# Kernel tuning notes

Measured on AMD Instinct MI355X. Metric: run time of the kernel, lower is better.

The kernel has to match this reference:

```python
import jax, jax.numpy as jnp
import numpy as np

KL_W = 0.001
DENSITY_W = 0.1
SIZING_W = 0.05
BIG = 1e6


def _pairwise_sqdist(x, y):
    # x: [B,N,3], y: [B,M,3] -> [B,N,M] squared euclidean distances
    x2 = jnp.sum(x * x, axis=-1)  # [B,N]
    y2 = jnp.sum(y * y, axis=-1)  # [B,M]
    xy = jnp.einsum('bnd,bmd->bnm', x, y)
    return x2[:, :, None] + y2[:, None, :] - 2.0 * xy


def setup_inputs() -> dict:
    key = jax.random.key(0)
    ks = jax.random.split(key, 6)
    B, N, D, L = 4, 4096, 3, 512
    return {
        'pred_pos': jax.random.normal(ks[0], (B, N, D), dtype=jnp.float32),
        'pred_sizing': jax.random.uniform(ks[1], (B, N), dtype=jnp.float32),
        'target_pos': jax.random.normal(ks[2], (B, N, D), dtype=jnp.float32),
        'target_sizing': jax.random.uniform(ks[3], (B, N), dtype=jnp.float32),
        'mu': jax.random.normal(ks[4], (B, L), dtype=jnp.float32),
        'logvar': jax.random.normal(ks[5], (B, L), dtype=jnp.float32),
    }


def reference(pred_pos, pred_sizing, target_pos, target_sizing, mu, logvar):
    # Chamfer distance (bidirectional)
    dist = _pairwise_sqdist(pred_pos, target_pos)  # [B,N,M]
    d_p2t = jnp.min(dist, axis=2).mean(axis=1)     # [B]
    d_t2p = jnp.min(dist, axis=1).mean(axis=1)     # [B]
    cd = jnp.mean(d_p2t + d_t2p)

    # KL divergence term
    kl = -0.5 * jnp.mean(1.0 + logvar - mu * mu - jnp.exp(logvar))

    # Density uniformity: std (ddof=1, torch default) of nearest-neighbor sq-dist
    N = pred_pos.shape[1]
    d_self = _pairwise_sqdist(pred_pos, pred_pos)
    d_self = d_self + jnp.eye(N, dtype=d_self.dtype)[None] * BIG
    nn_d = jnp.min(d_self, axis=2)                 # [B,N]
    density = jnp.mean(jnp.std(nn_d, axis=1, ddof=1))

    # Sizing MSE
    sizing = jnp.mean((pred_sizing - target_sizing) ** 2)

    total = cd + KL_W * kl + DENSITY_W * density + SIZING_W * sizing
    return total
```

## Files before the change

kernel.cpp:

```cpp
#include <hip/hip_runtime.h>
#include <cfloat>
#include <cmath>

#define NB     4
#define NPTS   4096
#define NLAT   512
#define RPTS   8
#define CJ     64
#define NJC    (NPTS / CJ)
#define NIH    2

__global__ __launch_bounds__(256) void k_prep(
    const float* __restrict__ pred_pos, const float* __restrict__ targ_pos,
    float4* __restrict__ predT, float4* __restrict__ predR,
    float4* __restrict__ targT, float4* __restrict__ targR)
{
    const int i = blockIdx.x * 256 + threadIdx.x;
    {
        const float x = pred_pos[3*i], y = pred_pos[3*i+1], z = pred_pos[3*i+2];
        const float p2 = fmaf(z, z, fmaf(y, y, x * x));
        predT[i] = make_float4(-2.f*x, -2.f*y, -2.f*z, p2);
        predR[i] = make_float4(x, y, z, p2);
    }
    {
        const float x = targ_pos[3*i], y = targ_pos[3*i+1], z = targ_pos[3*i+2];
        const float p2 = fmaf(z, z, fmaf(y, y, x * x));
        targT[i] = make_float4(-2.f*x, -2.f*y, -2.f*z, p2);
        targR[i] = make_float4(x, y, z, p2);
    }
}

__global__ __launch_bounds__(256) void k_min_dist(
    const float4* __restrict__ predT, const float4* __restrict__ predR,
    const float4* __restrict__ targT, const float4* __restrict__ targR,
    float* __restrict__ part_mins )
{
    __shared__ float4 lds[CJ];

    const int tid   = threadIdx.x;
    const int jc    = blockIdx.x & (NJC - 1);
    const int ihalf = (blockIdx.x >> 6) & 1;
    const int b     = (blockIdx.x >> 7) & 3;
    const int mode  = blockIdx.x >> 9;

    const float4* iR = ((mode == 1) ? targR : predR) + (size_t)b * NPTS;
    const float4* jT = ((mode == 0) ? targT : predT) + (size_t)b * NPTS + jc * CJ;

    if (tid < CJ) lds[tid] = jT[tid];

    float px[RPTS], py[RPTS], pz[RPTS], p2[RPTS], acc[RPTS];
    #pragma unroll
    for (int k = 0; k < RPTS; ++k) {
        const float4 r = iR[ihalf * 2048 + (k << 8) + tid];
        px[k] = r.x; py[k] = r.y; pz[k] = r.z; p2[k] = r.w;
        acc[k] = FLT_MAX;
    }
    __syncthreads();

    if (mode != 2) {
        #pragma unroll 2
        for (int j = 0; j < CJ; j += 2) {
            const float4 o1 = lds[j];
            const float4 o2 = lds[j + 1];
            #pragma unroll
            for (int k = 0; k < RPTS; ++k) {
                float t1 = fmaf(o1.x, px[k], o1.w);
                t1 = fmaf(o1.y, py[k], t1);
                t1 = fmaf(o1.z, pz[k], t1);
                float t2 = fmaf(o2.x, px[k], o2.w);
                t2 = fmaf(o2.y, py[k], t2);
                t2 = fmaf(o2.z, pz[k], t2);
                acc[k] = fminf(acc[k], fminf(t1, t2));
            }
        }
    } else {
        const bool have = (jc >> 5) == ihalf;
        const int  kself = (jc & 31) >> 2;
        const bool aff   = have && ((tid >> 6) == (jc & 3));
        const int  jself = tid & 63;
        float sx = px[0], sy = py[0], sz = pz[0];
        #pragma unroll
        for (int k = 1; k < RPTS; ++k) {
            sx = (k == kself) ? px[k] : sx;
            sy = (k == kself) ? py[k] : sy;
            sz = (k == kself) ? pz[k] : sz;
        }
        float accf = FLT_MAX;
        #pragma unroll 2
        for (int j = 0; j < CJ; j += 2) {
            const float4 o1 = lds[j];
            const float4 o2 = lds[j + 1];
            #pragma unroll
            for (int k = 0; k < RPTS; ++k) {
                float t1 = fmaf(o1.x, px[k], o1.w);
                t1 = fmaf(o1.y, py[k], t1);
                t1 = fmaf(o1.z, pz[k], t1);
                float t2 = fmaf(o2.x, px[k], o2.w);
                t2 = fmaf(o2.y, py[k], t2);
                t2 = fmaf(o2.z, pz[k], t2);
                acc[k] = fminf(acc[k], fminf(t1, t2));
            }
            float f1 = fmaf(o1.x, sx, o1.w);
            f1 = fmaf(o1.y, sy, f1);
            f1 = fmaf(o1.z, sz, f1);
            f1 = (j == jself) ? FLT_MAX : f1;
            float f2 = fmaf(o2.x, sx, o2.w);
            f2 = fmaf(o2.y, sy, f2);
            f2 = fmaf(o2.z, sz, f2);
            f2 = ((j + 1) == jself) ? FLT_MAX : f2;
            accf = fminf(accf, fminf(f1, f2));
        }
        #pragma unroll
        for (int k = 0; k < RPTS; ++k)
            acc[k] = (aff && k == kself) ? accf : acc[k];
    }

    float* mb = part_mins + (((size_t)mode * NB + b) * NJC + jc) * NPTS
                + ihalf * 2048;
    #pragma unroll
    for (int k = 0; k < RPTS; ++k)
        mb[(k << 8) + tid] = acc[k] + p2[k];
}

__device__ __forceinline__ float block_sum(float v, float* red)
{
    #pragma unroll
    for (int o = 32; o >= 1; o >>= 1) v += __shfl_xor(v, o);
    const int w = threadIdx.x >> 6;
    __syncthreads();
    if ((threadIdx.x & 63) == 0) red[w] = v;
    __syncthreads();
    return red[0] + red[1] + red[2] + red[3];
}

__global__ __launch_bounds__(256) void k_fold(
    const float* __restrict__ part_mins,
    const float* __restrict__ pred_sizing,
    const float* __restrict__ targ_sizing,
    const float* __restrict__ mu,
    const float* __restrict__ logvar,
    float* __restrict__ sums ,
    float* __restrict__ sumsqs )
{
    __shared__ float red[4];
    const int blk = blockIdx.x, tid = threadIdx.x;

    if (blk < 192) {
        const int slice = blk & 15;
        const int b     = (blk >> 4) & 3;
        const int mode  = blk >> 6;
        const float* base = part_mins + ((size_t)mode * NB + b) * NJC * NPTS
                            + slice * 256 + tid;
        float m = FLT_MAX;
        #pragma unroll 8
        for (int jc = 0; jc < NJC; ++jc)
            m = fminf(m, base[(size_t)jc * NPTS]);
        const float s  = block_sum(m, red);
        const float s2 = block_sum(m * m, red);
        if (tid == 0) { sums[blk] = s; sumsqs[blk] = s2; }
    } else if (blk == 192) {
        float kls = 0.f;
        for (int i = tid; i < NB * NLAT; i += 256) {
            const float lv = logvar[i], m = mu[i];
            kls += 1.f + lv - m * m - expf(lv);
        }
        kls = block_sum(kls, red);
        if (tid == 0) { sums[192] = kls; sumsqs[192] = 0.f; }
    } else {
        const float4* ps = (const float4*)pred_sizing;
        const float4* ts = (const float4*)targ_sizing;
        float szs = 0.f;
        #pragma unroll 4
        for (int i = tid; i < NB * NPTS / 4; i += 256) {
            const float4 a = ps[i], c = ts[i];
            const float d0 = a.x - c.x, d1 = a.y - c.y;
            const float d2 = a.z - c.z, d3 = a.w - c.w;
            szs += fmaf(d0, d0, fmaf(d1, d1, fmaf(d2, d2, d3 * d3)));
        }
        szs = block_sum(szs, red);
        if (tid == 0) { sums[193] = szs; sumsqs[193] = 0.f; }
    }
}

__global__ __launch_bounds__(256) void k_finalize(
    const float* __restrict__ sums, const float* __restrict__ sumsqs,
    float* __restrict__ out)
{
    __shared__ float gs[12], gq[12];
    const int t = threadIdx.x;

    float v = 0.f, v2 = 0.f;
    if (t < 192) { v = sums[t]; v2 = sumsqs[t]; }
    #pragma unroll
    for (int o = 1; o < 16; o <<= 1) {
        v  += __shfl_xor(v,  o);
        v2 += __shfl_xor(v2, o);
    }
    if (t < 192 && (t & 15) == 0) { gs[t >> 4] = v; gq[t >> 4] = v2; }
    __syncthreads();

    if (t == 0) {
        float cd = 0.f, dens = 0.f;
        for (int b = 0; b < NB; ++b) {
            const float s01 = gs[b] + gs[4 + b];
            const float sS  = gs[8 + b];
            const float sS2 = gq[8 + b];
            cd += s01 / (float)NPTS;
            const float var = (sS2 - sS * sS / (float)NPTS) / (float)(NPTS - 1);
            dens += sqrtf(fmaxf(var, 0.f));
        }
        cd   /= (float)NB;
        dens /= (float)NB;
        const float kl     = -0.5f * sums[192] / (float)(NB * NLAT);
        const float sizing = sums[193] / (float)(NB * NPTS);
        out[0] = cd + 0.001f * kl + 0.1f * dens + 0.05f * sizing;
    }
}

extern "C" void kernel_launch(void* const* d_in, const int* in_sizes, int n_in,
                              void* d_out, int out_size, void* d_ws, size_t ws_size,
                              hipStream_t stream)
{
    const float* pred_pos    = (const float*)d_in[0];
    const float* pred_sizing = (const float*)d_in[1];
    const float* targ_pos    = (const float*)d_in[2];
    const float* targ_sizing = (const float*)d_in[3];
    const float* mu          = (const float*)d_in[4];
    const float* logvar      = (const float*)d_in[5];

    float4* predT = (float4*)d_ws;
    float4* predR = predT + (size_t)NB * NPTS;
    float4* targT = predR + (size_t)NB * NPTS;
    float4* targR = targT + (size_t)NB * NPTS;
    float*  part_mins = (float*)(targR + (size_t)NB * NPTS);
    float*  sums   = part_mins + (size_t)3 * NB * NJC * NPTS;
    float*  sumsqs = sums + 194;

    k_prep<<<dim3(NB * NPTS / 256), dim3(256), 0, stream>>>(
        pred_pos, targ_pos, predT, predR, targT, targR);
    k_min_dist<<<dim3(3 * NB * NIH * NJC), dim3(256), 0, stream>>>(
        predT, predR, targT, targR, part_mins);
    k_fold<<<dim3(194), dim3(256), 0, stream>>>(
        part_mins, pred_sizing, targ_sizing, mu, logvar, sums, sumsqs);
    k_finalize<<<dim3(1), dim3(256), 0, stream>>>(sums, sumsqs, (float*)d_out);
}
```

Baseline: 47.73 us.

## Rotate j-points across lanes with DPP instead of LDS broadcast

```diff
diff --git a/kernel.cpp b/kernel.cpp
--- a/kernel.cpp
+++ b/kernel.cpp
@@ -5,10 +5,15 @@
 #define NB     4
 #define NPTS   4096
 #define NLAT   512
-#define RPTS   8
+#define RPTS   16
 #define CJ     64
 #define NJC    (NPTS / CJ)
-#define NIH    2
+
+__device__ __forceinline__ float dpp_ror1(float v)
+{
+    return __int_as_float(__builtin_amdgcn_mov_dpp(
+        __float_as_int(v), 0x13C , 0xF, 0xF, true));
+}
 
 __global__ __launch_bounds__(256) void k_prep(
     const float* __restrict__ pred_pos, const float* __restrict__ targ_pos,
@@ -35,88 +40,69 @@
     const float4* __restrict__ targT, const float4* __restrict__ targR,
     float* __restrict__ part_mins )
 {
-    __shared__ float4 lds[CJ];
-
-    const int tid   = threadIdx.x;
-    const int jc    = blockIdx.x & (NJC - 1);
-    const int ihalf = (blockIdx.x >> 6) & 1;
-    const int b     = (blockIdx.x >> 7) & 3;
-    const int mode  = blockIdx.x >> 9;
+    const int tid  = threadIdx.x;
+    const int lane = tid & 63;
+    const int w    = tid >> 6;
+    const int jc   = blockIdx.x & (NJC - 1);
+    const int b    = (blockIdx.x >> 6) & 3;
+    const int mode = blockIdx.x >> 8;
 
     const float4* iR = ((mode == 1) ? targR : predR) + (size_t)b * NPTS;
     const float4* jT = ((mode == 0) ? targT : predT) + (size_t)b * NPTS + jc * CJ;
 
-    if (tid < CJ) lds[tid] = jT[tid];
+    const float4 ja = jT[lane];
+    const float4 jb = jT[lane ^ 32];
+    float j1x = ja.x, j1y = ja.y, j1z = ja.z, j1w = ja.w;
+    float j2x = jb.x, j2y = jb.y, j2z = jb.z, j2w = jb.w;
 
     float px[RPTS], py[RPTS], pz[RPTS], p2[RPTS], acc[RPTS];
     #pragma unroll
     for (int k = 0; k < RPTS; ++k) {
-        const float4 r = iR[ihalf * 2048 + (k << 8) + tid];
+        const float4 r = iR[(k << 8) + tid];
         px[k] = r.x; py[k] = r.y; pz[k] = r.z; p2[k] = r.w;
         acc[k] = FLT_MAX;
     }
-    __syncthreads();
-
-    if (mode != 2) {
-        #pragma unroll 2
-        for (int j = 0; j < CJ; j += 2) {
-            const float4 o1 = lds[j];
-            const float4 o2 = lds[j + 1];
-            #pragma unroll
-            for (int k = 0; k < RPTS; ++k) {
-                float t1 = fmaf(o1.x, px[k], o1.w);
-                t1 = fmaf(o1.y, py[k], t1);
-                t1 = fmaf(o1.z, pz[k], t1);
-                float t2 = fmaf(o2.x, px[k], o2.w);
-                t2 = fmaf(o2.y, py[k], t2);
-                t2 = fmaf(o2.z, pz[k], t2);
-                acc[k] = fminf(acc[k], fminf(t1, t2));
-            }
-        }
-    } else {
-        const bool have = (jc >> 5) == ihalf;
-        const int  kself = (jc & 31) >> 2;
-        const bool aff   = have && ((tid >> 6) == (jc & 3));
-        const int  jself = tid & 63;
-        float sx = px[0], sy = py[0], sz = pz[0];
+
+    {
+        const int  d     = jc - w;
+        const bool skipw = (mode == 2) && (d >= 0) && ((d & 3) == 0);
+        const int  kself = d >> 2;
         #pragma unroll
-        for (int k = 1; k < RPTS; ++k) {
-            sx = (k == kself) ? px[k] : sx;
-            sy = (k == kself) ? py[k] : sy;
-            sz = (k == kself) ? pz[k] : sz;
-        }
-        float accf = FLT_MAX;
-        #pragma unroll 2
-        for (int j = 0; j < CJ; j += 2) {
-            const float4 o1 = lds[j];
-            const float4 o2 = lds[j + 1];
-            #pragma unroll
-            for (int k = 0; k < RPTS; ++k) {
-                float t1 = fmaf(o1.x, px[k], o1.w);
-                t1 = fmaf(o1.y, py[k], t1);
-                t1 = fmaf(o1.z, pz[k], t1);
-                float t2 = fmaf(o2.x, px[k], o2.w);
-                t2 = fmaf(o2.y, py[k], t2);
-                t2 = fmaf(o2.z, pz[k], t2);
-                acc[k] = fminf(acc[k], fminf(t1, t2));
-            }
-            float f1 = fmaf(o1.x, sx, o1.w);
-            f1 = fmaf(o1.y, sy, f1);
-            f1 = fmaf(o1.z, sz, f1);
-            f1 = (j == jself) ? FLT_MAX : f1;
-            float f2 = fmaf(o2.x, sx, o2.w);
-            f2 = fmaf(o2.y, sy, f2);
-            f2 = fmaf(o2.z, sz, f2);
-            f2 = ((j + 1) == jself) ? FLT_MAX : f2;
-            accf = fminf(accf, fminf(f1, f2));
-        }
+        for (int k = 0; k < RPTS; ++k) {
+            float t1 = fmaf(j1x, px[k], j1w);
+            t1 = fmaf(j1y, py[k], t1);
+            t1 = fmaf(j1z, pz[k], t1);
+            t1 = (skipw && k == kself) ? FLT_MAX : t1;
+            float t2 = fmaf(j2x, px[k], j2w);
+            t2 = fmaf(j2y, py[k], t2);
+            t2 = fmaf(j2z, pz[k], t2);
+            acc[k] = fminf(acc[k], fminf(t1, t2));
+        }
+        j1x = dpp_ror1(j1x); j1y = dpp_ror1(j1y);
+        j1z = dpp_ror1(j1z); j1w = dpp_ror1(j1w);
+        j2x = dpp_ror1(j2x); j2y = dpp_ror1(j2y);
+        j2z = dpp_ror1(j2z); j2w = dpp_ror1(j2w);
+    }
+
+    #pragma unroll 4
+    for (int s = 1; s < 32; ++s) {
         #pragma unroll
-        for (int k = 0; k < RPTS; ++k)
-            acc[k] = (aff && k == kself) ? accf : acc[k];
-    }
-
-    float* mb = part_mins + (((size_t)mode * NB + b) * NJC + jc) * NPTS
-                + ihalf * 2048;
+        for (int k = 0; k < RPTS; ++k) {
+            float t1 = fmaf(j1x, px[k], j1w);
+            t1 = fmaf(j1y, py[k], t1);
+            t1 = fmaf(j1z, pz[k], t1);
+            float t2 = fmaf(j2x, px[k], j2w);
+            t2 = fmaf(j2y, py[k], t2);
+            t2 = fmaf(j2z, pz[k], t2);
+            acc[k] = fminf(acc[k], fminf(t1, t2));
+        }
+        j1x = dpp_ror1(j1x); j1y = dpp_ror1(j1y);
+        j1z = dpp_ror1(j1z); j1w = dpp_ror1(j1w);
+        j2x = dpp_ror1(j2x); j2y = dpp_ror1(j2y);
+        j2z = dpp_ror1(j2z); j2w = dpp_ror1(j2w);
+    }
+
+    float* mb = part_mins + (((size_t)mode * NB + b) * NJC + jc) * NPTS;
     #pragma unroll
     for (int k = 0; k < RPTS; ++k)
         mb[(k << 8) + tid] = acc[k] + p2[k];
@@ -238,7 +224,7 @@
 
     k_prep<<<dim3(NB * NPTS / 256), dim3(256), 0, stream>>>(
         pred_pos, targ_pos, predT, predR, targT, targR);
-    k_min_dist<<<dim3(3 * NB * NIH * NJC), dim3(256), 0, stream>>>(
+    k_min_dist<<<dim3(3 * NB * NJC), dim3(256), 0, stream>>>(
         predT, predR, targT, targR, part_mins);
     k_fold<<<dim3(194), dim3(256), 0, stream>>>(
         part_mins, pred_sizing, targ_sizing, mu, logvar, sums, sumsqs);
```

After: 51.97 us. +8.9%, slower.

## Fuse prep into distance kernel and finalize into fold via atomic last-block

Applied to the files above, without the earlier changes.

```diff
diff --git a/kernel.cpp b/kernel.cpp
--- a/kernel.cpp
+++ b/kernel.cpp
@@ -5,54 +5,43 @@
 #define NB     4
 #define NPTS   4096
 #define NLAT   512
-#define RPTS   8
+#define RPTS   16
 #define CJ     64
 #define NJC    (NPTS / CJ)
-#define NIH    2
-
-__global__ __launch_bounds__(256) void k_prep(
-    const float* __restrict__ pred_pos, const float* __restrict__ targ_pos,
-    float4* __restrict__ predT, float4* __restrict__ predR,
-    float4* __restrict__ targT, float4* __restrict__ targR)
-{
-    const int i = blockIdx.x * 256 + threadIdx.x;
-    {
-        const float x = pred_pos[3*i], y = pred_pos[3*i+1], z = pred_pos[3*i+2];
-        const float p2 = fmaf(z, z, fmaf(y, y, x * x));
-        predT[i] = make_float4(-2.f*x, -2.f*y, -2.f*z, p2);
-        predR[i] = make_float4(x, y, z, p2);
-    }
-    {
-        const float x = targ_pos[3*i], y = targ_pos[3*i+1], z = targ_pos[3*i+2];
-        const float p2 = fmaf(z, z, fmaf(y, y, x * x));
-        targT[i] = make_float4(-2.f*x, -2.f*y, -2.f*z, p2);
-        targR[i] = make_float4(x, y, z, p2);
-    }
-}
-
-__global__ __launch_bounds__(256) void k_min_dist(
-    const float4* __restrict__ predT, const float4* __restrict__ predR,
-    const float4* __restrict__ targT, const float4* __restrict__ targR,
-    float* __restrict__ part_mins )
+#define NBLK   (3 * NB * NJC)
+#define NSUM   194
+
+__global__ __launch_bounds__(256, 4) void k_min_dist(
+    const float* __restrict__ pred_pos,
+    const float* __restrict__ targ_pos,
+    float* __restrict__ part_mins ,
+    unsigned int* __restrict__ counter)
 {
     __shared__ float4 lds[CJ];
 
-    const int tid   = threadIdx.x;
-    const int jc    = blockIdx.x & (NJC - 1);
-    const int ihalf = (blockIdx.x >> 6) & 1;
-    const int b     = (blockIdx.x >> 7) & 3;
-    const int mode  = blockIdx.x >> 9;
-
-    const float4* iR = ((mode == 1) ? targR : predR) + (size_t)b * NPTS;
-    const float4* jT = ((mode == 0) ? targT : predT) + (size_t)b * NPTS + jc * CJ;
-
-    if (tid < CJ) lds[tid] = jT[tid];
-
-    float px[RPTS], py[RPTS], pz[RPTS], p2[RPTS], acc[RPTS];
+    const int tid  = threadIdx.x;
+    const int jc   = blockIdx.x & (NJC - 1);
+    const int b    = (blockIdx.x >> 6) & 3;
+    const int mode = blockIdx.x >> 8;
+
+    if (blockIdx.x == 0 && tid == 0) *counter = 0u;
+
+    const float* pts = (mode == 1) ? targ_pos : pred_pos;
+    const float* oth = (mode == 0) ? targ_pos : pred_pos;
+
+    if (tid < CJ) {
+        const float* ob = oth + ((size_t)b * NPTS + jc * CJ) * 3;
+        const float x = ob[3 * tid], y = ob[3 * tid + 1], z = ob[3 * tid + 2];
+        const float o2 = fmaf(z, z, fmaf(y, y, x * x));
+        lds[tid] = make_float4(-2.f * x, -2.f * y, -2.f * z, o2);
+    }
+
+    const float* pb = pts + (size_t)b * NPTS * 3;
+    float px[RPTS], py[RPTS], pz[RPTS], acc[RPTS];
     #pragma unroll
     for (int k = 0; k < RPTS; ++k) {
-        const float4 r = iR[ihalf * 2048 + (k << 8) + tid];
-        px[k] = r.x; py[k] = r.y; pz[k] = r.z; p2[k] = r.w;
+        const float* pp = pb + 3 * (tid + (k << 8));
+        px[k] = pp[0]; py[k] = pp[1]; pz[k] = pp[2];
         acc[k] = FLT_MAX;
     }
     __syncthreads();
@@ -74,9 +63,8 @@
             }
         }
     } else {
-        const bool have = (jc >> 5) == ihalf;
-        const int  kself = (jc & 31) >> 2;
-        const bool aff   = have && ((tid >> 6) == (jc & 3));
+        const int  kself = jc >> 2;
+        const bool aff   = (tid >> 6) == (jc & 3);
         const int  jself = tid & 63;
         float sx = px[0], sy = py[0], sz = pz[0];
         #pragma unroll
@@ -115,11 +103,12 @@
             acc[k] = (aff && k == kself) ? accf : acc[k];
     }
 
-    float* mb = part_mins + (((size_t)mode * NB + b) * NJC + jc) * NPTS
-                + ihalf * 2048;
-    #pragma unroll
-    for (int k = 0; k < RPTS; ++k)
-        mb[(k << 8) + tid] = acc[k] + p2[k];
+    float* mb = part_mins + (((size_t)mode * NB + b) * NJC + jc) * NPTS;
+    #pragma unroll
+    for (int k = 0; k < RPTS; ++k) {
+        const float p2 = fmaf(pz[k], pz[k], fmaf(py[k], py[k], px[k] * px[k]));
+        mb[tid + (k << 8)] = acc[k] + p2;
+    }
 }
 
 __device__ __forceinline__ float block_sum(float v, float* red)
@@ -133,16 +122,20 @@
     return red[0] + red[1] + red[2] + red[3];
 }
 
-__global__ __launch_bounds__(256) void k_fold(
+__global__ __launch_bounds__(256) void k_fold_final(
     const float* __restrict__ part_mins,
     const float* __restrict__ pred_sizing,
     const float* __restrict__ targ_sizing,
     const float* __restrict__ mu,
     const float* __restrict__ logvar,
     float* __restrict__ sums ,
-    float* __restrict__ sumsqs )
+    float* __restrict__ sumsqs ,
+    unsigned int* __restrict__ counter,
+    float* __restrict__ out)
 {
     __shared__ float red[4];
+    __shared__ float gs[12], gq[12];
+    __shared__ unsigned int elect;
     const int blk = blockIdx.x, tid = threadIdx.x;
 
     if (blk < 192) {
@@ -180,26 +173,27 @@
         szs = block_sum(szs, red);
         if (tid == 0) { sums[193] = szs; sumsqs[193] = 0.f; }
     }
-}
-
-__global__ __launch_bounds__(256) void k_finalize(
-    const float* __restrict__ sums, const float* __restrict__ sumsqs,
-    float* __restrict__ out)
-{
-    __shared__ float gs[12], gq[12];
-    const int t = threadIdx.x;
+
+    __syncthreads();
+    if (tid == 0) {
+        __threadfence();
+        elect = (atomicAdd(counter, 1u) == (unsigned)(NSUM - 1));
+    }
+    __syncthreads();
+    if (!elect) return;
+    __threadfence();
 
     float v = 0.f, v2 = 0.f;
-    if (t < 192) { v = sums[t]; v2 = sumsqs[t]; }
+    if (tid < 192) { v = sums[tid]; v2 = sumsqs[tid]; }
     #pragma unroll
     for (int o = 1; o < 16; o <<= 1) {
         v  += __shfl_xor(v,  o);
         v2 += __shfl_xor(v2, o);
     }
-    if (t < 192 && (t & 15) == 0) { gs[t >> 4] = v; gq[t >> 4] = v2; }
-    __syncthreads();
-
-    if (t == 0) {
+    if (tid < 192 && (tid & 15) == 0) { gs[tid >> 4] = v; gq[tid >> 4] = v2; }
+    __syncthreads();
+
+    if (tid == 0) {
         float cd = 0.f, dens = 0.f;
         for (int b = 0; b < NB; ++b) {
             const float s01 = gs[b] + gs[4 + b];
@@ -228,19 +222,14 @@
     const float* mu          = (const float*)d_in[4];
     const float* logvar      = (const float*)d_in[5];
 
-    float4* predT = (float4*)d_ws;
-    float4* predR = predT + (size_t)NB * NPTS;
-    float4* targT = predR + (size_t)NB * NPTS;
-    float4* targR = targT + (size_t)NB * NPTS;
-    float*  part_mins = (float*)(targR + (size_t)NB * NPTS);
-    float*  sums   = part_mins + (size_t)3 * NB * NJC * NPTS;
-    float*  sumsqs = sums + 194;
-
-    k_prep<<<dim3(NB * NPTS / 256), dim3(256), 0, stream>>>(
-        pred_pos, targ_pos, predT, predR, targT, targR);
-    k_min_dist<<<dim3(3 * NB * NIH * NJC), dim3(256), 0, stream>>>(
-        predT, predR, targT, targR, part_mins);
-    k_fold<<<dim3(194), dim3(256), 0, stream>>>(
-        part_mins, pred_sizing, targ_sizing, mu, logvar, sums, sumsqs);
-    k_finalize<<<dim3(1), dim3(256), 0, stream>>>(sums, sumsqs, (float*)d_out);
-}
+    float* part_mins = (float*)d_ws;
+    float* sums      = part_mins + (size_t)3 * NB * NJC * NPTS;
+    float* sumsqs    = sums + NSUM;
+    unsigned int* counter = (unsigned int*)(sumsqs + NSUM);
+
+    k_min_dist<<<dim3(NBLK), dim3(256), 0, stream>>>(
+        pred_pos, targ_pos, part_mins, counter);
+    k_fold_final<<<dim3(NSUM), dim3(256), 0, stream>>>(
+        part_mins, pred_sizing, targ_sizing, mu, logvar,
+        sums, sumsqs, counter, (float*)d_out);
+}
```

After: 46.79 us. -2.0%, faster.
